# Kernel optimization log

Measured on AMD Instinct MI355X. Metric: run time of the kernel, lower is better.

## Reference

```python
import jax, jax.numpy as jnp
import numpy as np

# --- QTIP TCQ config (matches init_kwargs) ---
M, K = 4096, 4096          # out_features, in_features
TD_X, TD_Y = 16, 16        # tile dims
L = 16                     # trellis state bits
KV = 4                     # bits consumed per step (K=2 bits/weight * V=2)
V = 2                      # weights emitted per step
TLUT_BITS = 9              # lut index bits
T_STEPS = TD_X * TD_Y // V # 128 steps per tile
NBITS = T_STEPS * KV       # 512 bits per tile (tail-biting: exactly K bits/weight)
NWORDS = NBITS // 16       # 32 int16 words per tile
NT = (M // TD_X) * (K // TD_Y)  # 65536 tiles
BATCH, SEQ = 4, 2048


def setup_inputs() -> dict:
    key = jax.random.key(0)
    k1, k2, k3 = jax.random.split(key, 3)
    inp = jax.random.normal(k1, (BATCH, SEQ, K), dtype=jnp.float32)
    # int16 buffer modeled as int32 holding arbitrary 16-bit patterns
    trellis = jax.random.randint(k2, (NT, NWORDS), 0, 65536, dtype=jnp.int32)
    tlut = jax.random.normal(k3, (2 ** TLUT_BITS, V), dtype=jnp.float32) * 0.02
    return {"inp": inp, "trellis": trellis, "tlut": tlut}


def _decode(trellis, tlut):
    """Decode bit-packed tail-biting bitshift trellis codes into dense W [M, K]."""
    words = trellis.astype(jnp.uint32) & 0xFFFF          # uint16 bit patterns
    shifts = (15 - jnp.arange(16)).astype(jnp.uint32)    # MSB-first within word
    bits = ((words[:, :, None] >> shifts) & 1).astype(jnp.int32).reshape(NT, NBITS)
    # step t reads L-bit window starting at t*KV, wrapping around (tail-biting)
    win = (jnp.arange(T_STEPS)[:, None] * KV + jnp.arange(L)[None, :]) % NBITS  # [T, L]
    bw = bits[:, win]                                    # [NT, T, L]
    pow2 = (2 ** (L - 1 - jnp.arange(L))).astype(jnp.int32)
    state = jnp.einsum('ntl,l->nt', bw, pow2)            # L-bit state per step
    code = state & (2 ** TLUT_BITS - 1)                  # low tlut_bits index the lut
    w = tlut[code].reshape(NT, TD_X, TD_Y)               # V outputs/step, row-major tile
    # tiles are laid out row-major over (M//td_x, K//td_y)
    w = w.reshape(M // TD_X, K // TD_Y, TD_X, TD_Y).transpose(0, 2, 1, 3).reshape(M, K)
    return w


def reference(inp, trellis, tlut):
    Wd = _decode(trellis, tlut)          # [M, K]
    x = inp.reshape(-1, K)               # [bs, K]
    y = x @ Wd.T                         # [bs, M]
    return y.reshape(*inp.shape[:-1], M).astype(inp.dtype)
```

## Files before the change

### kernel.cpp

```cpp
#include <hip/hip_runtime.h>
#include <hip/hip_bf16.h>

#define AS1 __attribute__((address_space(1)))
#define AS3 __attribute__((address_space(3)))

typedef __bf16 bf16x8 __attribute__((ext_vector_type(8)));
typedef float f32x4 __attribute__((ext_vector_type(4)));

#define GLOAD_LDS16(gptr, lptr) \
  __builtin_amdgcn_global_load_lds((AS1 void*)(gptr), (AS3 void*)(lptr), 16, 0, 0)

#define M_W   4096
#define K_DIM 4096
#define M_X   8192
#define NT_T  65536
#define TSTEPS 128
#define NKT   (K_DIM/64)

#define BAR()    __builtin_amdgcn_s_barrier()
#define SCHED0() __builtin_amdgcn_sched_barrier(0)
#define VM6()    asm volatile("s_waitcnt vmcnt(6)" ::: "memory")
#define VM0()    asm volatile("s_waitcnt vmcnt(0)" ::: "memory")

__device__ __forceinline__ unsigned short f2bf(float f) {
  unsigned int u = __float_as_uint(f);
  unsigned int r = (u + 0x7FFFu + ((u >> 16) & 1u)) >> 16;
  return (unsigned short)r;
}

__global__ void cvt_kernel(const float* __restrict__ x, unsigned short* __restrict__ xb) {
  int idx = blockIdx.x * blockDim.x + threadIdx.x;
  const float4* p = reinterpret_cast<const float4*>(x) + (size_t)idx * 2;
  float4 u = p[0];
  float4 v = p[1];
  uint4 o;
  o.x = (unsigned)f2bf(u.x) | ((unsigned)f2bf(u.y) << 16);
  o.y = (unsigned)f2bf(u.z) | ((unsigned)f2bf(u.w) << 16);
  o.z = (unsigned)f2bf(v.x) | ((unsigned)f2bf(v.y) << 16);
  o.w = (unsigned)f2bf(v.z) | ((unsigned)f2bf(v.w) << 16);
  reinterpret_cast<uint4*>(xb)[idx] = o;
}

__global__ void decode_kernel(const int* __restrict__ trellis,
                              const float* __restrict__ tlut,
                              unsigned short* __restrict__ W) {
  int idx = blockIdx.x * blockDim.x + threadIdx.x;
  int t = idx >> 7;
  int s = idx & 127;
  const unsigned int* tr = reinterpret_cast<const unsigned int*>(trellis) + t * 32;
  int w0  = s >> 2;
  int off = (s & 3) * 4;
  unsigned int a = tr[w0] & 0xFFFFu;
  unsigned int state;
  if (off == 0) {
    state = a;
  } else {
    unsigned int b = tr[(w0 + 1) & 31] & 0xFFFFu;
    state = ((a << off) | (b >> (16 - off))) & 0xFFFFu;
  }
  unsigned int code = state & 0x1FFu;
  float2 v = reinterpret_cast<const float2*>(tlut)[code];
  int i = t >> 8;
  int j = t & 255;
  int flat = s * 2;
  int r = flat >> 4;
  int c = flat & 15;
  unsigned int packed = (unsigned)f2bf(v.x) | ((unsigned)f2bf(v.y) << 16);
  size_t o = (size_t)(i * 16 + r) * K_DIM + (j * 16 + c);
  *reinterpret_cast<unsigned int*>(W + o) = packed;
}


template<int SB>
__device__ __forceinline__ void lda2(const char* ldsc, int a0, int a1, bf16x8 af[4][2]) {
  #pragma unroll
  for (int fm = 0; fm < 4; ++fm) {
    af[fm][0] = *(const bf16x8*)(ldsc + SB + fm * 2048 + a0);
    af[fm][1] = *(const bf16x8*)(ldsc + SB + fm * 2048 + a1);
  }
}

template<int SB>
__device__ __forceinline__ void ldb2(const char* ldsc, int b0, int b1, bf16x8 bq[2][2]) {
  #pragma unroll
  for (int fn = 0; fn < 2; ++fn) {
    bq[fn][0] = *(const bf16x8*)(ldsc + SB + fn * 2048 + b0);
    bq[fn][1] = *(const bf16x8*)(ldsc + SB + fn * 2048 + b1);
  }
}

template<int MH, int NH>
__device__ __forceinline__ void mmq(const bf16x8 af[4][2], const bf16x8 bq[2][2],
                                    f32x4 acc[8][4]) {
  __builtin_amdgcn_s_setprio(1);
  #pragma unroll
  for (int kh = 0; kh < 2; ++kh)
    #pragma unroll
    for (int fm = 0; fm < 4; ++fm)
      #pragma unroll
      for (int fn = 0; fn < 2; ++fn)
        acc[MH * 4 + fm][NH * 2 + fn] =
            __builtin_amdgcn_mfma_f32_16x16x32_bf16(af[fm][kh], bq[fn][kh],
                                                    acc[MH * 4 + fm][NH * 2 + fn], 0, 0, 0);
  __builtin_amdgcn_s_setprio(0);
}

template<int BUF, int HALF>
__device__ __forceinline__ void stA(const unsigned short* xb, char* ldsc, int kt,
                                    int gArow0, int gArow1, int gcol, int lo0) {
  const unsigned short* s0 = xb + (size_t)(gArow0 + HALF * 64) * K_DIM + kt * 64 + gcol;
  const unsigned short* s1 = xb + (size_t)(gArow1 + HALF * 64) * K_DIM + kt * 64 + gcol;
  GLOAD_LDS16(s0, ldsc + (BUF * 2 + HALF) * 16384 + lo0);
  GLOAD_LDS16(s1, ldsc + (BUF * 2 + HALF) * 16384 + lo0 + 1024);
}

template<int BUF, int HALF>
__device__ __forceinline__ void stB(const unsigned short* W, char* ldsc, int kt,
                                    int gBrow0, int gBrow1, int gcol, int lo0) {
  const unsigned short* s0 = W + (size_t)(gBrow0 + HALF * 32) * K_DIM + kt * 64 + gcol;
  const unsigned short* s1 = W + (size_t)(gBrow1 + HALF * 32) * K_DIM + kt * 64 + gcol;
  GLOAD_LDS16(s0, ldsc + 65536 + (BUF * 2 + HALF) * 16384 + lo0);
  GLOAD_LDS16(s1, ldsc + 65536 + (BUF * 2 + HALF) * 16384 + lo0 + 1024);
}

__global__ __launch_bounds__(512, 2) void gemm8_kernel(const unsigned short* __restrict__ xb,
                                                       const unsigned short* __restrict__ W,
                                                       float* __restrict__ y) {
  extern __shared__ __align__(16) char ldsc[];

  int bid = blockIdx.x;
  int swz = (bid & 7) * 64 + (bid >> 3);
  int brow = (swz >> 4) * 256;
  int bcol = (swz & 15) * 256;

  int tid  = threadIdx.x;
  int lane = tid & 63;
  int wid  = tid >> 6;
  int wr = wid >> 2;
  int wc = wid & 3;

  int lr = lane >> 4, la7 = lane & 7, lc = lane & 15;
  int k0 = (lr ^ la7) << 4;
  int k1 = ((4 + lr) ^ la7) << 4;
  int a0 = (wr * 64 + lc) * 128 + k0;
  int a1 = (wr * 64 + lc) * 128 + k1;
  int b0 = (wc * 32 + lc) * 128 + k0;
  int b1 = (wc * 32 + lc) * 128 + k1;

  int q0 = wid * 16 + (lane >> 3);
  int q1 = q0 + 8;
  int lo0 = wid * 2048 + lane * 16;
  int gcol = ((lane & 7) ^ (lane >> 3)) << 3;
  int gArow0 = brow + (q0 >> 6) * 128 + (q0 & 63);
  int gArow1 = brow + (q1 >> 6) * 128 + (q1 & 63);
  int gBrow0 = bcol + (q0 >> 5) * 64 + (q0 & 31);
  int gBrow1 = bcol + (q1 >> 5) * 64 + (q1 & 31);

  f32x4 acc[8][4];
  #pragma unroll
  for (int m = 0; m < 8; ++m)
    #pragma unroll
    for (int n = 0; n < 4; ++n)
      acc[m][n] = (f32x4){0.f, 0.f, 0.f, 0.f};

  bf16x8 afA[4][2], afB[4][2];
  bf16x8 bqX[2][2], bqY[2][2];

  stA<0,0>(xb, ldsc, 0, gArow0, gArow1, gcol, lo0);
  stB<0,0>(W,  ldsc, 0, gBrow0, gBrow1, gcol, lo0);
  stB<0,1>(W,  ldsc, 0, gBrow0, gBrow1, gcol, lo0);
  stA<0,1>(xb, ldsc, 0, gArow0, gArow1, gcol, lo0);
  stA<1,0>(xb, ldsc, 1, gArow0, gArow1, gcol, lo0);
  stB<1,0>(W,  ldsc, 1, gBrow0, gBrow1, gcol, lo0);
  stB<1,1>(W,  ldsc, 1, gBrow0, gBrow1, gcol, lo0);
  VM0(); BAR();

  lda2<0 * 16384>(ldsc, a0, a1, afA);
  ldb2<65536 + 0 * 16384>(ldsc, b0, b1, bqX);

  #pragma unroll 1
  for (int i = 0; i < NKT / 2; ++i) {
    int t1 = 2 * i + 1;
    int t2 = 2 * i + 2; if (t2 > NKT - 1) t2 = NKT - 1;
    int t3 = 2 * i + 3; if (t3 > NKT - 1) t3 = NKT - 1;

    lda2<1 * 16384>(ldsc, a0, a1, afB);
    stA<1,1>(xb, ldsc, t1, gArow0, gArow1, gcol, lo0);
    SCHED0();
    mmq<0,0>(afA, bqX, acc);
    VM6(); BAR();

    ldb2<65536 + 1 * 16384>(ldsc, b0, b1, bqY);
    stA<0,0>(xb, ldsc, t2, gArow0, gArow1, gcol, lo0);
    SCHED0();
    mmq<1,0>(afB, bqX, acc);
    VM6(); BAR();

    stB<0,0>(W, ldsc, t2, gBrow0, gBrow1, gcol, lo0);
    SCHED0();
    mmq<1,1>(afB, bqY, acc);
    VM6(); BAR();

    lda2<2 * 16384>(ldsc, a0, a1, afB);
    ldb2<65536 + 2 * 16384>(ldsc, b0, b1, bqX);
    stB<0,1>(W, ldsc, t2, gBrow0, gBrow1, gcol, lo0);
    SCHED0();
    mmq<0,1>(afA, bqY, acc);
    VM6(); BAR();

    lda2<3 * 16384>(ldsc, a0, a1, afA);
    stA<0,1>(xb, ldsc, t2, gArow0, gArow1, gcol, lo0);
    SCHED0();
    mmq<0,0>(afB, bqX, acc);
    VM6(); BAR();

    ldb2<65536 + 3 * 16384>(ldsc, b0, b1, bqY);
    stA<1,0>(xb, ldsc, t3, gArow0, gArow1, gcol, lo0);
    SCHED0();
    mmq<1,0>(afA, bqX, acc);
    VM6(); BAR();

    stB<1,0>(W, ldsc, t3, gBrow0, gBrow1, gcol, lo0);
    SCHED0();
    mmq<1,1>(afA, bqY, acc);
    VM6(); BAR();

    lda2<0 * 16384>(ldsc, a0, a1, afA);
    ldb2<65536 + 0 * 16384>(ldsc, b0, b1, bqX);
    stB<1,1>(W, ldsc, t3, gBrow0, gBrow1, gcol, lo0);
    SCHED0();
    mmq<0,1>(afB, bqY, acc);
    VM6(); BAR();
  }

  VM0();

  #pragma unroll
  for (int am = 0; am < 8; ++am) {
    #pragma unroll
    for (int an = 0; an < 4; ++an) {
      int row0 = brow + wr * 128 + am * 16 + (lane >> 4) * 4;
      int col  = bcol + wc * 64 + an * 16 + (lane & 15);
      #pragma unroll
      for (int j = 0; j < 4; ++j)
        y[(size_t)(row0 + j) * M_W + col] = acc[am][an][j];
    }
  }
}

extern "C" void kernel_launch(void* const* d_in, const int* in_sizes, int n_in,
                              void* d_out, int out_size, void* d_ws, size_t ws_size,
                              hipStream_t stream) {
  const float* inp     = (const float*)d_in[0];
  const int*   trellis = (const int*)d_in[1];
  const float* tlut    = (const float*)d_in[2];
  float* y = (float*)d_out;

  unsigned short* xb = (unsigned short*)d_ws;
  unsigned short* Wd = (unsigned short*)((char*)d_ws + (size_t)M_X * K_DIM * 2);

  (void)hipFuncSetAttribute((const void*)gemm8_kernel,
                            hipFuncAttributeMaxDynamicSharedMemorySize, 131072);

  cvt_kernel<<<M_X * K_DIM / 8 / 256, 256, 0, stream>>>(inp, xb);
  decode_kernel<<<NT_T * TSTEPS / 256, 256, 0, stream>>>(trellis, tlut, Wd);
  gemm8_kernel<<<dim3(512), dim3(512), 131072, stream>>>(xb, Wd, y);
}
```

Measured before the change: 283.9 us.

## Switch GEMM main loop to 32x32x16 MFMA with per-k-half LDS fragment schedule

Replaces the 16x16x32 bf16 MFMA tiles with 32x32x16 MFMA tiles. This roughly halves the number of MFMA issues and lowers LDS fragment reads per FLOP. It restructures the 8-phase loop so each phase loads A and B fragments for one k-half, then waits on lgkmcnt and a barrier before the MFMAs. The vmcnt wait depths and the output store mapping are retuned to match. The cost is that LDS reads are no longer prefetched ahead of the MFMAs, and the extra barriers each phase can expose LDS latency.

```diff
diff --git a/kernel.cpp b/kernel.cpp
--- a/kernel.cpp
+++ b/kernel.cpp
@@ -5,7 +5,7 @@
 #define AS3 __attribute__((address_space(3)))
 
 typedef __bf16 bf16x8 __attribute__((ext_vector_type(8)));
-typedef float f32x4 __attribute__((ext_vector_type(4)));
+typedef float f32x16 __attribute__((ext_vector_type(16)));
 
 #define GLOAD_LDS16(gptr, lptr) \
   __builtin_amdgcn_global_load_lds((AS1 void*)(gptr), (AS3 void*)(lptr), 16, 0, 0)
@@ -17,10 +17,9 @@
 #define TSTEPS 128
 #define NKT   (K_DIM/64)
 
-#define BAR()    __builtin_amdgcn_s_barrier()
-#define SCHED0() __builtin_amdgcn_sched_barrier(0)
-#define VM6()    asm volatile("s_waitcnt vmcnt(6)" ::: "memory")
-#define VM0()    asm volatile("s_waitcnt vmcnt(0)" ::: "memory")
+#define BAR()        __builtin_amdgcn_s_barrier()
+#define WAIT_LGKM0() asm volatile("s_waitcnt lgkmcnt(0)" ::: "memory")
+#define VMW(n)       asm volatile("s_waitcnt vmcnt(" #n ")" ::: "memory")
 
 __device__ __forceinline__ unsigned short f2bf(float f) {
   unsigned int u = __float_as_uint(f);
@@ -71,37 +70,40 @@
 }
 
 
-template<int SB>
-__device__ __forceinline__ void lda2(const char* ldsc, int a0, int a1, bf16x8 af[4][2]) {
-  #pragma unroll
-  for (int fm = 0; fm < 4; ++fm) {
-    af[fm][0] = *(const bf16x8*)(ldsc + SB + fm * 2048 + a0);
-    af[fm][1] = *(const bf16x8*)(ldsc + SB + fm * 2048 + a1);
-  }
-}
-
-template<int SB>
-__device__ __forceinline__ void ldb2(const char* ldsc, int b0, int b1, bf16x8 bq[2][2]) {
-  #pragma unroll
-  for (int fn = 0; fn < 2; ++fn) {
-    bq[fn][0] = *(const bf16x8*)(ldsc + SB + fn * 2048 + b0);
-    bq[fn][1] = *(const bf16x8*)(ldsc + SB + fn * 2048 + b1);
-  }
-}
-
-template<int MH, int NH>
-__device__ __forceinline__ void mmq(const bf16x8 af[4][2], const bf16x8 bq[2][2],
-                                    f32x4 acc[8][4]) {
+template<int BUF, int MH, int KH>
+__device__ __forceinline__ void ldAq(const char* ldsc, int r0, int r1, const int* kc,
+                                     bf16x8 av[2][2]) {
+  const char* s = ldsc + (BUF * 2 + MH) * 16384;
+  av[0][0] = *(const bf16x8*)(s + r0 + kc[2 * KH + 0]);
+  av[0][1] = *(const bf16x8*)(s + r0 + kc[2 * KH + 1]);
+  av[1][0] = *(const bf16x8*)(s + r1 + kc[2 * KH + 0]);
+  av[1][1] = *(const bf16x8*)(s + r1 + kc[2 * KH + 1]);
+}
+
+template<int BUF, int KH>
+__device__ __forceinline__ void ldBq(const char* ldsc, int br, const int* kc,
+                                     bf16x8 bh[2][4]) {
+  const char* s0 = ldsc + 65536 + (BUF * 2 + 0) * 16384;
+  const char* s1 = ldsc + 65536 + (BUF * 2 + 1) * 16384;
+  bh[0][2 * KH + 0] = *(const bf16x8*)(s0 + br + kc[2 * KH + 0]);
+  bh[0][2 * KH + 1] = *(const bf16x8*)(s0 + br + kc[2 * KH + 1]);
+  bh[1][2 * KH + 0] = *(const bf16x8*)(s1 + br + kc[2 * KH + 0]);
+  bh[1][2 * KH + 1] = *(const bf16x8*)(s1 + br + kc[2 * KH + 1]);
+}
+
+template<int MH, int KH>
+__device__ __forceinline__ void mm32(const bf16x8 av[2][2], const bf16x8 bh[2][4],
+                                     f32x16 (&acc)[4][2]) {
   __builtin_amdgcn_s_setprio(1);
   #pragma unroll
-  for (int kh = 0; kh < 2; ++kh)
+  for (int kk = 0; kk < 2; ++kk)
     #pragma unroll
-    for (int fm = 0; fm < 4; ++fm)
+    for (int j = 0; j < 2; ++j)
       #pragma unroll
-      for (int fn = 0; fn < 2; ++fn)
-        acc[MH * 4 + fm][NH * 2 + fn] =
-            __builtin_amdgcn_mfma_f32_16x16x32_bf16(af[fm][kh], bq[fn][kh],
-                                                    acc[MH * 4 + fm][NH * 2 + fn], 0, 0, 0);
+      for (int nf = 0; nf < 2; ++nf)
+        acc[2 * MH + j][nf] =
+            __builtin_amdgcn_mfma_f32_32x32x16_bf16(av[j][kk], bh[nf][2 * KH + kk],
+                                                    acc[2 * MH + j][nf], 0, 0, 0);
   __builtin_amdgcn_s_setprio(0);
 }
 
@@ -139,13 +141,13 @@
   int wr = wid >> 2;
   int wc = wid & 3;
 
-  int lr = lane >> 4, la7 = lane & 7, lc = lane & 15;
-  int k0 = (lr ^ la7) << 4;
-  int k1 = ((4 + lr) ^ la7) << 4;
-  int a0 = (wr * 64 + lc) * 128 + k0;
-  int a1 = (wr * 64 + lc) * 128 + k1;
-  int b0 = (wc * 32 + lc) * 128 + k0;
-  int b1 = (wc * 32 + lc) * 128 + k1;
+  int l31 = lane & 31, la7 = lane & 7, hi = lane >> 5;
+  int kc[4];
+  #pragma unroll
+  for (int ks = 0; ks < 4; ++ks) kc[ks] = ((2 * ks + hi) ^ la7) << 4;
+  int aR0 = (wr * 64 + 0 * 32 + l31) * 128;
+  int aR1 = (wr * 64 + 1 * 32 + l31) * 128;
+  int bR  = (wc * 32 + l31) * 128;
 
   int q0 = wid * 16 + (lane >> 3);
   int q1 = q0 + 8;
@@ -156,27 +158,26 @@
   int gBrow0 = bcol + (q0 >> 5) * 64 + (q0 & 31);
   int gBrow1 = bcol + (q1 >> 5) * 64 + (q1 & 31);
 
-  f32x4 acc[8][4];
-  #pragma unroll
-  for (int m = 0; m < 8; ++m)
+  f32x16 acc[4][2];
+  #pragma unroll
+  for (int m = 0; m < 4; ++m)
     #pragma unroll
-    for (int n = 0; n < 4; ++n)
-      acc[m][n] = (f32x4){0.f, 0.f, 0.f, 0.f};
-
-  bf16x8 afA[4][2], afB[4][2];
-  bf16x8 bqX[2][2], bqY[2][2];
+    for (int n = 0; n < 2; ++n)
+      #pragma unroll
+      for (int e = 0; e < 16; ++e)
+        acc[m][n][e] = 0.f;
+
+  bf16x8 av[2][2];
+  bf16x8 bh[2][4];
 
   stA<0,0>(xb, ldsc, 0, gArow0, gArow1, gcol, lo0);
+  stA<0,1>(xb, ldsc, 0, gArow0, gArow1, gcol, lo0);
   stB<0,0>(W,  ldsc, 0, gBrow0, gBrow1, gcol, lo0);
   stB<0,1>(W,  ldsc, 0, gBrow0, gBrow1, gcol, lo0);
-  stA<0,1>(xb, ldsc, 0, gArow0, gArow1, gcol, lo0);
   stA<1,0>(xb, ldsc, 1, gArow0, gArow1, gcol, lo0);
   stB<1,0>(W,  ldsc, 1, gBrow0, gBrow1, gcol, lo0);
   stB<1,1>(W,  ldsc, 1, gBrow0, gBrow1, gcol, lo0);
-  VM0(); BAR();
-
-  lda2<0 * 16384>(ldsc, a0, a1, afA);
-  ldb2<65536 + 0 * 16384>(ldsc, b0, b1, bqX);
+  VMW(0); BAR();
 
   #pragma unroll 1
   for (int i = 0; i < NKT / 2; ++i) {
@@ -184,66 +185,74 @@
     int t2 = 2 * i + 2; if (t2 > NKT - 1) t2 = NKT - 1;
     int t3 = 2 * i + 3; if (t3 > NKT - 1) t3 = NKT - 1;
 
-    lda2<1 * 16384>(ldsc, a0, a1, afB);
+    ldAq<0,0,0>(ldsc, aR0, aR1, kc, av);
+    ldBq<0,0>(ldsc, bR, kc, bh);
     stA<1,1>(xb, ldsc, t1, gArow0, gArow1, gcol, lo0);
-    SCHED0();
-    mmq<0,0>(afA, bqX, acc);
-    VM6(); BAR();
-
-    ldb2<65536 + 1 * 16384>(ldsc, b0, b1, bqY);
+    BAR(); WAIT_LGKM0();
+    mm32<0,0>(av, bh, acc);
+    VMW(10); BAR();
+
+    ldAq<0,0,1>(ldsc, aR0, aR1, kc, av);
+    ldBq<0,1>(ldsc, bR, kc, bh);
+    BAR(); WAIT_LGKM0();
+    mm32<0,1>(av, bh, acc);
+    VMW(8); BAR();
+
+    ldAq<0,1,1>(ldsc, aR0, aR1, kc, av);
     stA<0,0>(xb, ldsc, t2, gArow0, gArow1, gcol, lo0);
-    SCHED0();
-    mmq<1,0>(afB, bqX, acc);
-    VM6(); BAR();
-
-    stB<0,0>(W, ldsc, t2, gBrow0, gBrow1, gcol, lo0);
-    SCHED0();
-    mmq<1,1>(afB, bqY, acc);
-    VM6(); BAR();
-
-    lda2<2 * 16384>(ldsc, a0, a1, afB);
-    ldb2<65536 + 2 * 16384>(ldsc, b0, b1, bqX);
+    stB<0,0>(W,  ldsc, t2, gBrow0, gBrow1, gcol, lo0);
+    BAR(); WAIT_LGKM0();
+    mm32<1,1>(av, bh, acc);
+    VMW(12); BAR();
+
+    ldAq<0,1,0>(ldsc, aR0, aR1, kc, av);
     stB<0,1>(W, ldsc, t2, gBrow0, gBrow1, gcol, lo0);
-    SCHED0();
-    mmq<0,1>(afA, bqY, acc);
-    VM6(); BAR();
-
-    lda2<3 * 16384>(ldsc, a0, a1, afA);
+    BAR(); WAIT_LGKM0();
+    mm32<1,0>(av, bh, acc);
+    VMW(8); BAR();
+
+    ldAq<1,0,0>(ldsc, aR0, aR1, kc, av);
+    ldBq<1,0>(ldsc, bR, kc, bh);
     stA<0,1>(xb, ldsc, t2, gArow0, gArow1, gcol, lo0);
-    SCHED0();
-    mmq<0,0>(afB, bqX, acc);
-    VM6(); BAR();
-
-    ldb2<65536 + 3 * 16384>(ldsc, b0, b1, bqY);
+    BAR(); WAIT_LGKM0();
+    mm32<0,0>(av, bh, acc);
+    VMW(10); BAR();
+
+    ldAq<1,0,1>(ldsc, aR0, aR1, kc, av);
+    ldBq<1,1>(ldsc, bR, kc, bh);
+    BAR(); WAIT_LGKM0();
+    mm32<0,1>(av, bh, acc);
+    VMW(8); BAR();
+
+    ldAq<1,1,1>(ldsc, aR0, aR1, kc, av);
     stA<1,0>(xb, ldsc, t3, gArow0, gArow1, gcol, lo0);
-    SCHED0();
-    mmq<1,0>(afA, bqX, acc);
-    VM6(); BAR();
-
-    stB<1,0>(W, ldsc, t3, gBrow0, gBrow1, gcol, lo0);
-    SCHED0();
-    mmq<1,1>(afA, bqY, acc);
-    VM6(); BAR();
-
-    lda2<0 * 16384>(ldsc, a0, a1, afA);
-    ldb2<65536 + 0 * 16384>(ldsc, b0, b1, bqX);
+    stB<1,0>(W,  ldsc, t3, gBrow0, gBrow1, gcol, lo0);
+    BAR(); WAIT_LGKM0();
+    mm32<1,1>(av, bh, acc);
+    VMW(12); BAR();
+
+    ldAq<1,1,0>(ldsc, aR0, aR1, kc, av);
     stB<1,1>(W, ldsc, t3, gBrow0, gBrow1, gcol, lo0);
-    SCHED0();
-    mmq<0,1>(afB, bqY, acc);
-    VM6(); BAR();
+    BAR(); WAIT_LGKM0();
+    mm32<1,0>(av, bh, acc);
+    VMW(8); BAR();
   }
 
-  VM0();
-
-  #pragma unroll
-  for (int am = 0; am < 8; ++am) {
+  VMW(0);
+
+  #pragma unroll
+  for (int mf = 0; mf < 4; ++mf) {
     #pragma unroll
-    for (int an = 0; an < 4; ++an) {
-      int row0 = brow + wr * 128 + am * 16 + (lane >> 4) * 4;
-      int col  = bcol + wc * 64 + an * 16 + (lane & 15);
+    for (int nf = 0; nf < 2; ++nf) {
+      int col = bcol + wc * 64 + nf * 32 + l31;
+      int rb  = brow + wr * 128 + mf * 32 + 4 * hi;
       #pragma unroll
-      for (int j = 0; j < 4; ++j)
-        y[(size_t)(row0 + j) * M_W + col] = acc[am][an][j];
+      for (int g = 0; g < 4; ++g) {
+        #pragma unroll
+        for (int e = 0; e < 4; ++e) {
+          y[(size_t)(rb + g * 8 + e) * M_W + col] = acc[mf][nf][g * 4 + e];
+        }
+      }
     }
   }
 }
```

Result: slower. 308.8 us (+8.8%).
